# Kernel optimization log

Measured on AMD Instinct MI355X. Metric: run time of the kernel, lower is better.

## Reference

```python
import jax, jax.numpy as jnp
import numpy as np

N = 100000


def gcn_conv(x, W, b, src, dst, deg_inv_sqrt, n):
    # PyG GCNConv: h = D^{-1/2} (A + I) D^{-1/2} (x W) + b
    h = x @ W  # [N, out]
    norm = deg_inv_sqrt[src] * deg_inv_sqrt[dst]  # [E+N]
    msgs = h[src] * norm[:, None]  # gathered + scaled messages
    out = jax.ops.segment_sum(msgs, dst, num_segments=n)
    return out + b


def _self_loops_and_norm(edge_index, n):
    src, dst = edge_index[0], edge_index[1]
    loop = jnp.arange(n, dtype=edge_index.dtype)
    src = jnp.concatenate([src, loop])
    dst = jnp.concatenate([dst, loop])
    deg = jax.ops.segment_sum(jnp.ones_like(dst, dtype=jnp.float32), dst, num_segments=n)
    deg_inv_sqrt = jnp.where(deg > 0, jax.lax.rsqrt(jnp.maximum(deg, 1.0)), 0.0)
    return src, dst, deg_inv_sqrt


def setup_inputs() -> dict:
    key = jax.random.key(0)
    k1, k2, k3, k4 = jax.random.split(key, 4)
    nfeat, nhid, nclass = 512, 256, 40
    E = 3200000
    x = jax.random.normal(k1, (N, nfeat), dtype=jnp.float32)
    edge_index = jax.random.randint(k2, (2, E), 0, N, dtype=jnp.int64)
    # Glorot-style init for GCNConv weights, zero bias (PyG default)
    W1 = jax.random.normal(k3, (nfeat, nhid), dtype=jnp.float32) / np.sqrt(nfeat)
    b1 = jnp.zeros((nhid,), dtype=jnp.float32)
    W2 = jax.random.normal(k4, (nhid, nclass), dtype=jnp.float32) / np.sqrt(nhid)
    b2 = jnp.zeros((nclass,), dtype=jnp.float32)
    return {"x": x, "W1": W1, "b1": b1, "W2": W2, "b2": b2, "edge_index": edge_index}


def reference(x, W1, b1, W2, b2, edge_index):
    src, dst, dis = _self_loops_and_norm(edge_index, N)
    h = gcn_conv(x, W1, b1, src, dst, dis, N)
    h = jax.nn.relu(h)
    # dropout(p=0.5) is identity in eval mode
    h = gcn_conv(h, W2, b2, src, dst, dis, N)
    return jax.nn.log_softmax(h, axis=1)
```

## Files before the change

### kernel.cpp

```cpp
#include <hip/hip_runtime.h>
#include <math.h>

#define NFEAT 512
#define NHID  256
#define NCLASS 40
#define NBUCK 782
#define BCAP  5120
#define PCHUNK 8192

typedef __attribute__((ext_vector_type(8))) short short8;
typedef __attribute__((ext_vector_type(4))) float f32x4;


__device__ __forceinline__ float bflo(unsigned u) {
    union { unsigned i; float f; } x; x.i = u << 16; return x.f;
}
__device__ __forceinline__ float bfhi(unsigned u) {
    union { unsigned i; float f; } x; x.i = u & 0xffff0000u; return x.f;
}
__device__ __forceinline__ unsigned short f2bf(float f) {
    union { float f; unsigned i; } x; x.f = f;
    unsigned r = x.i + 0x7fffu + ((x.i >> 16) & 1u);
    return (unsigned short)(r >> 16);
}
__device__ __forceinline__ float bf2f(unsigned short h) {
    union { unsigned i; float f; } x; x.i = (unsigned)h << 16; return x.f;
}
__device__ __forceinline__ unsigned pack2(float a, float b) {
    return (unsigned)f2bf(a) | ((unsigned)f2bf(b) << 16);
}


__global__ __launch_bounds__(256) void partcast_k(const float* __restrict__ W1,
                                                  unsigned short* __restrict__ WTsw,
                                                  const float* __restrict__ W2,
                                                  unsigned short* __restrict__ WT2,
                                                  const int* __restrict__ ei,
                                                  int* bucketCnt,
                                                  unsigned* __restrict__ binned, int E) {
    __shared__ unsigned staged[PCHUNK];
    __shared__ int hist[NBUCK];
    __shared__ int lofs[NBUCK];
    __shared__ int sbase[NBUCK];
    __shared__ int lcur[NBUCK];
    __shared__ int wsum[256];
    int bid = blockIdx.x;
    int t = threadIdx.x;
    if (bid < 64) {
        int tid = bid * 256 + t;
        int nn = tid >> 6;
        int k8 = tid & 63;
        unsigned short buf[8];
#pragma unroll
        for (int j = 0; j < 8; ++j)
            buf[j] = f2bf(W1[(size_t)(k8 * 8 + j) * NHID + nn]);
        size_t dst = ((size_t)((nn >> 4) * 16 + (k8 >> 2)) * 64 +
                      (k8 & 3) * 16 + (nn & 15)) * 8;
        *(uint4*)(WTsw + dst) = *(const uint4*)buf;
        return;
    }
    if (bid == 64) {
        for (int idx = t; idx < 96 * 256; idx += 256) {
            int j2 = idx >> 8;
            int k = idx & 255;
            int j = (j2 < 48) ? j2 : j2 - 48;
            float v = (j < NCLASS) ? W2[k * NCLASS + j] : 0.f;
            unsigned short hi = f2bf(v);
            WT2[idx] = (j2 < 48) ? hi : f2bf(v - bf2f(hi));
        }
        return;
    }
    int pb = bid - 65;
    int beg = pb * PCHUNK;
    int end = beg + PCHUNK; if (end > E) end = E;

    for (int b = t; b < NBUCK; b += 256) hist[b] = 0;
    __syncthreads();
    for (int e = beg + t; e < end; e += 256) {
        int d = ei[(size_t)E + e];
        atomicAdd(&hist[d >> 7], 1);
    }
    __syncthreads();
    int v[4];
    int s0 = 0;
#pragma unroll
    for (int r = 0; r < 4; ++r) {
        int idx = t * 4 + r;
        v[r] = (idx < NBUCK) ? hist[idx] : 0;
        s0 += v[r];
    }
    wsum[t] = s0;
    __syncthreads();
    for (int off = 1; off < 256; off <<= 1) {
        int add = (t >= off) ? wsum[t - off] : 0;
        __syncthreads();
        wsum[t] += add;
        __syncthreads();
    }
    int excl = wsum[t] - s0;
#pragma unroll
    for (int r = 0; r < 4; ++r) {
        int idx = t * 4 + r;
        if (idx < NBUCK) { lofs[idx] = excl; lcur[idx] = excl; }
        excl += v[r];
    }
    __syncthreads();
    for (int b = t; b < NBUCK; b += 256) {
        int h = hist[b];
        if (h) sbase[b] = atomicAdd(&bucketCnt[b], h);
    }
    for (int e = beg + t; e < end; e += 256) {
        int s = ei[e];
        int d = ei[(size_t)E + e];
        int b = d >> 7;
        int p = atomicAdd(&lcur[b], 1);
        staged[p] = ((unsigned)s << 7) | (unsigned)(d & 127);
    }
    __syncthreads();
    int w = t >> 6, lane = t & 63;
    for (int b = w; b < NBUCK; b += 4) {
        int h = hist[b];
        if (!h) continue;
        int lo = lofs[b];
        size_t gb = (size_t)b * BCAP + sbase[b];
        for (int l = lane; l < h; l += 64)
            binned[gb + l] = staged[lo + l];
    }
}


__global__ __launch_bounds__(1024) void bscan_k(const int* __restrict__ bucketCnt,
                                                int* __restrict__ bbase,
                                                int* __restrict__ offs, int n, int E) {
    __shared__ int sd[1024];
    int t = threadIdx.x;
    int v = (t < NBUCK) ? bucketCnt[t] : 0;
    sd[t] = v;
    __syncthreads();
    for (int off = 1; off < 1024; off <<= 1) {
        int add = (t >= off) ? sd[t - off] : 0;
        __syncthreads();
        sd[t] += add;
        __syncthreads();
    }
    if (t < NBUCK) bbase[t] = sd[t] - v;
    if (t == 0) offs[n] = E;
}


__global__ __launch_bounds__(512) void fill2_k(const unsigned* __restrict__ binned,
                                               const int* __restrict__ bucketCnt,
                                               const int* __restrict__ bbase,
                                               int* __restrict__ offs,
                                               float* __restrict__ dis,
                                               int* __restrict__ csrs, int n) {
    __shared__ int h128[128];
    __shared__ int sd[128];
    __shared__ int lcur[128];
    int b = blockIdx.x;
    int t = threadIdx.x;
    int node0 = b << 7;
    int cbt = bucketCnt[b];
    size_t base_in = (size_t)b * BCAP;
    int gbase = bbase[b];
    if (t < 128) h128[t] = 0;
    __syncthreads();
    for (int e = t; e < cbt; e += 512) {
        unsigned u = binned[base_in + e];
        atomicAdd(&h128[u & 127], 1);
    }
    __syncthreads();
    int v = (t < 128) ? h128[t] : 0;
    if (t < 128) sd[t] = v;
    __syncthreads();
    for (int off = 1; off < 128; off <<= 1) {
        int add = (t < 128 && t >= off) ? sd[t - off] : 0;
        __syncthreads();
        if (t < 128) sd[t] += add;
        __syncthreads();
    }
    if (t < 128) {
        int excl = sd[t] - v;
        int nd = node0 + t;
        if (nd < n) {
            offs[nd] = gbase + excl;
            dis[nd] = rsqrtf((float)v + 1.0f);
        }
        lcur[t] = gbase + excl;
    }
    __syncthreads();
    for (int e = t; e < cbt; e += 512) {
        unsigned u = binned[base_in + e];
        int pos = atomicAdd(&lcur[u & 127], 1);
        csrs[pos] = (int)(u >> 7);
    }
}


__global__ __launch_bounds__(512) void gemm1_k(const float* __restrict__ X,
                                               const unsigned short* __restrict__ WTsw,
                                               const float* __restrict__ dis,
                                               unsigned short* __restrict__ H, int M) {
    __shared__ unsigned short as[128][72];
    int t = threadIdx.x;
    int lane = t & 63;
    int w = t >> 6;
    int wm = w >> 2;
    int wn = w & 3;
    int m0 = blockIdx.x * 128;
    int quad = lane >> 4;
    int r16 = lane & 15;

    f32x4 acc[4][4];
#pragma unroll
    for (int a = 0; a < 4; ++a)
#pragma unroll
        for (int b = 0; b < 4; ++b) acc[a][b] = (f32x4){0.f, 0.f, 0.f, 0.f};

    for (int k0 = 0; k0 < NFEAT; k0 += 64) {
        {
            int m = t >> 2;
            int c = (t & 3) * 16;
            int gi = m0 + m;
            float4 v0, v1, v2, v3;
            if (gi < M) {
                const float4* p = (const float4*)(X + (size_t)gi * NFEAT + k0 + c);
                v0 = p[0]; v1 = p[1]; v2 = p[2]; v3 = p[3];
            } else {
                v0 = v1 = v2 = v3 = make_float4(0.f, 0.f, 0.f, 0.f);
            }
            uint4 p0, p1;
            p0.x = pack2(v0.x, v0.y); p0.y = pack2(v0.z, v0.w);
            p0.z = pack2(v1.x, v1.y); p0.w = pack2(v1.z, v1.w);
            p1.x = pack2(v2.x, v2.y); p1.y = pack2(v2.z, v2.w);
            p1.z = pack2(v3.x, v3.y); p1.w = pack2(v3.z, v3.w);
            *(uint4*)&as[m][c] = p0;
            *(uint4*)&as[m][c + 8] = p1;
        }
        __syncthreads();
        int kb0 = k0 >> 5;
#pragma unroll
        for (int ks = 0; ks < 2; ++ks) {
            int kblk = kb0 + ks;
            short8 af[4], bfr[4];
#pragma unroll
            for (int sm = 0; sm < 4; ++sm)
                af[sm] = *(const short8*)&as[wm * 64 + sm * 16 + r16][ks * 32 + quad * 8];
#pragma unroll
            for (int sn = 0; sn < 4; ++sn)
                bfr[sn] = *(const short8*)(WTsw +
                    ((size_t)((wn * 4 + sn) * 16 + kblk) * 64 + lane) * 8);
#pragma unroll
            for (int sm = 0; sm < 4; ++sm)
#pragma unroll
                for (int sn = 0; sn < 4; ++sn)
                    acc[sm][sn] = __builtin_amdgcn_mfma_f32_16x16x32_bf16(
                        af[sm], bfr[sn], acc[sm][sn], 0, 0, 0);
        }
        __syncthreads();
    }
#pragma unroll
    for (int sm = 0; sm < 4; ++sm) {
#pragma unroll
        for (int rr = 0; rr < 4; ++rr) {
            int row = m0 + wm * 64 + sm * 16 + quad * 4 + rr;
            if (row < M) {
                float dsc = dis[row];
#pragma unroll
                for (int sn = 0; sn < 4; ++sn) {
                    int col = wn * 64 + sn * 16 + r16;
                    H[(size_t)row * NHID + col] = f2bf(acc[sm][sn][rr] * dsc);
                }
            }
        }
    }
}


__global__ __launch_bounds__(256) void agg1h_k(const unsigned short* __restrict__ Hb,
                                               const int* __restrict__ offs,
                                               const int* __restrict__ csrs,
                                               const float* __restrict__ dis,
                                               const float* __restrict__ b1,
                                               unsigned short* __restrict__ outb,
                                               int n, int f0u) {
    int lane = threadIdx.x & 63;
    int i = blockIdx.x * 4 + (threadIdx.x >> 6);
    if (i >= n) return;
    const unsigned* Hv = (const unsigned*)Hb;
    int col = f0u + lane;
    float a0 = 0.f, a1 = 0.f;
    int beg = offs[i], end = offs[i + 1];
    int e = beg;
    {
        int c[16]; unsigned g[16];
        for (; e + 16 <= end; e += 16) {
#pragma unroll
            for (int u = 0; u < 16; ++u) c[u] = csrs[e + u];
#pragma unroll
            for (int u = 0; u < 16; ++u) g[u] = Hv[(size_t)c[u] * 128 + col];
#pragma unroll
            for (int u = 0; u < 16; ++u) {
                a0 += bflo(g[u]); a1 += bfhi(g[u]);
            }
        }
        if (e < end) {
#pragma unroll
            for (int u = 0; u < 16; ++u)
                c[u] = (e + u < end) ? csrs[e + u] : i;
#pragma unroll
            for (int u = 0; u < 16; ++u) g[u] = Hv[(size_t)c[u] * 128 + col];
#pragma unroll
            for (int u = 0; u < 16; ++u) {
                float sel = (e + u < end) ? 1.f : 0.f;
                a0 = fmaf(sel, bflo(g[u]), a0); a1 = fmaf(sel, bfhi(g[u]), a1);
            }
        }
    }
    unsigned v = Hv[(size_t)i * 128 + col];
    a0 += bflo(v); a1 += bfhi(v);
    float di = dis[i];
    float2 bb = ((const float2*)b1)[col];
    a0 = fmaxf(fmaf(a0, di, bb.x), 0.f);
    a1 = fmaxf(fmaf(a1, di, bb.y), 0.f);
    ((unsigned*)outb)[(size_t)i * 128 + col] = pack2(a0, a1);
}


__global__ __launch_bounds__(256) void gemm2_k(const unsigned short* __restrict__ Ab,
                                               const unsigned short* __restrict__ WT2,
                                               const float* __restrict__ dis,
                                               unsigned short* __restrict__ H2b, int M) {
    __shared__ unsigned short wt2s[96][264];
    int t = threadIdx.x;
    int lane = t & 63;
    int w = t >> 6;
    int quad = lane >> 4;
    int r16 = lane & 15;
    for (int idx = t; idx < 96 * 32; idx += 256) {
        int r = idx >> 5;
        int c = idx & 31;
        *(uint4*)&wt2s[r][c * 8] = ((const uint4*)(WT2 + (size_t)r * 256))[c];
    }
    __syncthreads();
    int row0 = blockIdx.x * 64 + w * 16;
    int gr = row0 + r16;
    f32x4 acc[3];
#pragma unroll
    for (int sn = 0; sn < 3; ++sn) acc[sn] = (f32x4){0.f, 0.f, 0.f, 0.f};
#pragma unroll
    for (int ks = 0; ks < 8; ++ks) {
        short8 af;
        if (gr < M)
            af = *(const short8*)(Ab + (size_t)gr * NHID + ks * 32 + quad * 8);
        else
            af = (short8){0, 0, 0, 0, 0, 0, 0, 0};
#pragma unroll
        for (int sn = 0; sn < 3; ++sn) {
            short8 bhi = *(const short8*)&wt2s[sn * 16 + r16][ks * 32 + quad * 8];
            short8 blo = *(const short8*)&wt2s[48 + sn * 16 + r16][ks * 32 + quad * 8];
            acc[sn] = __builtin_amdgcn_mfma_f32_16x16x32_bf16(af, bhi, acc[sn], 0, 0, 0);
            acc[sn] = __builtin_amdgcn_mfma_f32_16x16x32_bf16(af, blo, acc[sn], 0, 0, 0);
        }
    }
#pragma unroll
    for (int rr = 0; rr < 4; ++rr) {
        int row = row0 + quad * 4 + rr;
        if (row < M) {
            float dsc = dis[row];
#pragma unroll
            for (int sn = 0; sn < 3; ++sn)
                H2b[(size_t)row * 64 + sn * 16 + r16] = f2bf(acc[sn][rr] * dsc);
        }
    }
    if (lane < 32) {
        int row = row0 + r16;
        if (row < M)
            *(uint4*)&H2b[(size_t)row * 64 + 48 + (lane >> 4) * 8] =
                make_uint4(0u, 0u, 0u, 0u);
    }
}


__global__ __launch_bounds__(256) void agg2_k(const unsigned short* __restrict__ H2b,
                                              const int* __restrict__ offs,
                                              const int* __restrict__ csrs,
                                              const float* __restrict__ dis,
                                              const float* __restrict__ b2,
                                              float* __restrict__ out, int n) {
    int lane = threadIdx.x & 63;
    int i = blockIdx.x * 4 + (threadIdx.x >> 6);
    if (i >= n) return;
    const uint2* Hv = (const uint2*)H2b;
    int slot = lane >> 4;
    int r16 = lane & 15;
    float a0 = 0.f, a1 = 0.f, a2 = 0.f, a3 = 0.f;
    int beg = offs[i], end = offs[i + 1];
    int e = beg;
    {
        int c[8]; uint2 g[8];
        for (; e + 32 <= end; e += 32) {
#pragma unroll
            for (int u = 0; u < 8; ++u) c[u] = csrs[e + u * 4 + slot];
#pragma unroll
            for (int u = 0; u < 8; ++u) g[u] = Hv[(size_t)c[u] * 16 + r16];
#pragma unroll
            for (int u = 0; u < 8; ++u) {
                a0 += bflo(g[u].x); a1 += bfhi(g[u].x);
                a2 += bflo(g[u].y); a3 += bfhi(g[u].y);
            }
        }
        if (e < end) {
#pragma unroll
            for (int u = 0; u < 8; ++u) {
                int idx = e + u * 4 + slot;
                c[u] = (idx < end) ? csrs[idx] : i;
            }
#pragma unroll
            for (int u = 0; u < 8; ++u) g[u] = Hv[(size_t)c[u] * 16 + r16];
#pragma unroll
            for (int u = 0; u < 8; ++u) {
                float sel = (e + u * 4 + slot < end) ? 1.f : 0.f;
                a0 = fmaf(sel, bflo(g[u].x), a0); a1 = fmaf(sel, bfhi(g[u].x), a1);
                a2 = fmaf(sel, bflo(g[u].y), a2); a3 = fmaf(sel, bfhi(g[u].y), a3);
            }
        }
    }
    if (slot == 0) {
        uint2 v = Hv[(size_t)i * 16 + r16];
        a0 += bflo(v.x); a1 += bfhi(v.x);
        a2 += bflo(v.y); a3 += bfhi(v.y);
    }
    a0 += __shfl_xor(a0, 16, 64); a0 += __shfl_xor(a0, 32, 64);
    a1 += __shfl_xor(a1, 16, 64); a1 += __shfl_xor(a1, 32, 64);
    a2 += __shfl_xor(a2, 16, 64); a2 += __shfl_xor(a2, 32, 64);
    a3 += __shfl_xor(a3, 16, 64); a3 += __shfl_xor(a3, 32, 64);
    float di = dis[i];
    bool act = (r16 < 10);
    float4 bb = act ? ((const float4*)b2)[r16] : make_float4(0.f, 0.f, 0.f, 0.f);
    a0 = fmaf(a0, di, bb.x); a1 = fmaf(a1, di, bb.y);
    a2 = fmaf(a2, di, bb.z); a3 = fmaf(a3, di, bb.w);
    float m = act ? fmaxf(fmaxf(a0, a1), fmaxf(a2, a3)) : -INFINITY;
#pragma unroll
    for (int off = 8; off > 0; off >>= 1) m = fmaxf(m, __shfl_xor(m, off, 16));
    float s = act ? (expf(a0 - m) + expf(a1 - m) + expf(a2 - m) + expf(a3 - m)) : 0.f;
#pragma unroll
    for (int off = 8; off > 0; off >>= 1) s += __shfl_xor(s, off, 16);
    float ls = m + logf(s);
    if (lane < 10) {
        float4 o = make_float4(a0 - ls, a1 - ls, a2 - ls, a3 - ls);
        ((float4*)(out + (size_t)i * NCLASS))[lane] = o;
    }
}


extern "C" void kernel_launch(void* const* d_in, const int* in_sizes, int n_in,
                              void* d_out, int out_size, void* d_ws, size_t ws_size,
                              hipStream_t stream) {
    const float* x  = (const float*)d_in[0];
    const float* W1 = (const float*)d_in[1];
    const float* b1 = (const float*)d_in[2];
    const float* W2 = (const float*)d_in[3];
    const float* b2 = (const float*)d_in[4];
    const int*   ei = (const int*)d_in[5];

    const int N = in_sizes[0] / NFEAT;
    const int E = in_sizes[5] / 2;

    size_t off = 0;
    auto alloc = [&](size_t bytes) { size_t o = off; off += (bytes + 255) & ~(size_t)255; return o; };
    char* ws = (char*)d_ws;
    int*            offs    = (int*)           (ws + alloc((size_t)(N + 1) * 4));
    float*          dis     = (float*)         (ws + alloc((size_t)N * 4));
    int*            bcnt    = (int*)           (ws + alloc((size_t)NBUCK * 4));
    int*            bbase   = (int*)           (ws + alloc((size_t)NBUCK * 4));
    unsigned*       binned  = (unsigned*)      (ws + alloc((size_t)NBUCK * BCAP * 4));
    int*            csrs    = (int*)           (ws + alloc((size_t)E * 4));
    unsigned short* wTsw    = (unsigned short*)(ws + alloc((size_t)NFEAT * NHID * 2));
    unsigned short* wT2     = (unsigned short*)(ws + alloc((size_t)96 * 256 * 2));
    unsigned short* h1b     = (unsigned short*)(ws + alloc((size_t)N * NHID * 2));
    unsigned short* a1b     = (unsigned short*)(ws + alloc((size_t)N * NHID * 2));
    unsigned short* h2b     = (unsigned short*)(ws + alloc((size_t)N * 64 * 2));
    float*          out     = (float*)d_out;

    int npart = (E + PCHUNK - 1) / PCHUNK;

    hipMemsetAsync(bcnt, 0, (size_t)NBUCK * 4, stream);
    partcast_k<<<65 + npart, 256, 0, stream>>>(W1, wTsw, W2, wT2, ei, bcnt, binned, E);
    bscan_k<<<1, 1024, 0, stream>>>(bcnt, bbase, offs, N, E);
    fill2_k<<<NBUCK, 512, 0, stream>>>(binned, bcnt, bbase, offs, dis, csrs, N);
    gemm1_k<<<(N + 127) / 128, 512, 0, stream>>>(x, wTsw, dis, h1b, N);
    agg1h_k<<<(N + 3) / 4, 256, 0, stream>>>(h1b, offs, csrs, dis, b1, a1b, N, 0);
    agg1h_k<<<(N + 3) / 4, 256, 0, stream>>>(h1b, offs, csrs, dis, b1, a1b, N, 64);
    gemm2_k<<<(N + 63) / 64, 256, 0, stream>>>(a1b, wT2, dis, h2b, N);
    agg2_k<<<(N + 3) / 4, 256, 0, stream>>>(h2b, offs, csrs, dis, b2, out, N);
}
```

Before: 710.5 us.

## Sub-sort CSR neighbors into source-index ranges for gather locality

The CSR build now splits each destination node's neighbor list into 8 source-index ranges (by src/12500), storing 8 offsets per node. The first-layer aggregation walks the ranges in order, so concurrent warps tend to gather from similar regions of H and get better L2/MALL locality. The cost is a larger offset array, extra per-range loop overhead with partial 8-wide tails in agg1, and a hardcoded 12500 divisor that assumes N=100000.

```diff
diff --git a/kernel.cpp b/kernel.cpp
--- a/kernel.cpp
+++ b/kernel.cpp
@@ -7,6 +7,7 @@
 #define NBUCK 782
 #define BCAP  5120
 #define PCHUNK 8192
+#define NRANGE 8
 
 typedef __attribute__((ext_vector_type(8))) short short8;
 typedef __attribute__((ext_vector_type(4))) float f32x4;
@@ -131,7 +132,7 @@
 
 __global__ __launch_bounds__(1024) void bscan_k(const int* __restrict__ bucketCnt,
                                                 int* __restrict__ bbase,
-                                                int* __restrict__ offs, int n, int E) {
+                                                int* __restrict__ offsR, int n, int E) {
     __shared__ int sd[1024];
     int t = threadIdx.x;
     int v = (t < NBUCK) ? bucketCnt[t] : 0;
@@ -144,55 +145,66 @@
         __syncthreads();
     }
     if (t < NBUCK) bbase[t] = sd[t] - v;
-    if (t == 0) offs[n] = E;
+    if (t == 0) offsR[(size_t)n * NRANGE] = E;
 }
 
 
 __global__ __launch_bounds__(512) void fill2_k(const unsigned* __restrict__ binned,
                                                const int* __restrict__ bucketCnt,
                                                const int* __restrict__ bbase,
-                                               int* __restrict__ offs,
+                                               int* __restrict__ offsR,
                                                float* __restrict__ dis,
                                                int* __restrict__ csrs, int n) {
-    __shared__ int h128[128];
-    __shared__ int sd[128];
-    __shared__ int lcur[128];
+    __shared__ int h[1024];
+    __shared__ int sd[512];
+    __shared__ int lcur[1024];
     int b = blockIdx.x;
     int t = threadIdx.x;
     int node0 = b << 7;
     int cbt = bucketCnt[b];
     size_t base_in = (size_t)b * BCAP;
     int gbase = bbase[b];
-    if (t < 128) h128[t] = 0;
+    h[t] = 0; h[t + 512] = 0;
     __syncthreads();
     for (int e = t; e < cbt; e += 512) {
         unsigned u = binned[base_in + e];
-        atomicAdd(&h128[u & 127], 1);
-    }
-    __syncthreads();
-    int v = (t < 128) ? h128[t] : 0;
-    if (t < 128) sd[t] = v;
-    __syncthreads();
-    for (int off = 1; off < 128; off <<= 1) {
-        int add = (t < 128 && t >= off) ? sd[t - off] : 0;
-        __syncthreads();
-        if (t < 128) sd[t] += add;
-        __syncthreads();
-    }
+        int s = (int)(u >> 7);
+        int r = s / 12500;
+        atomicAdd(&h[((u & 127) << 3) + r], 1);
+    }
+    __syncthreads();
+    int v0 = h[t * 2], v1 = h[t * 2 + 1];
+    int s2 = v0 + v1;
+    sd[t] = s2;
+    __syncthreads();
+    for (int off = 1; off < 512; off <<= 1) {
+        int add = (t >= off) ? sd[t - off] : 0;
+        __syncthreads();
+        sd[t] += add;
+        __syncthreads();
+    }
+    int excl = sd[t] - s2;
+    lcur[t * 2] = gbase + excl;
+    lcur[t * 2 + 1] = gbase + excl + v0;
+    __syncthreads();
+    offsR[(size_t)(node0 << 3) + t] = lcur[t];
+    offsR[(size_t)(node0 << 3) + t + 512] = lcur[t + 512];
     if (t < 128) {
-        int excl = sd[t] - v;
         int nd = node0 + t;
         if (nd < n) {
-            offs[nd] = gbase + excl;
-            dis[nd] = rsqrtf((float)v + 1.0f);
-        }
-        lcur[t] = gbase + excl;
+            int deg = 0;
+#pragma unroll
+            for (int r = 0; r < 8; ++r) deg += h[(t << 3) + r];
+            dis[nd] = rsqrtf((float)deg + 1.0f);
+        }
     }
     __syncthreads();
     for (int e = t; e < cbt; e += 512) {
         unsigned u = binned[base_in + e];
-        int pos = atomicAdd(&lcur[u & 127], 1);
-        csrs[pos] = (int)(u >> 7);
+        int s = (int)(u >> 7);
+        int r = s / 12500;
+        int pos = atomicAdd(&lcur[((u & 127) << 3) + r], 1);
+        csrs[pos] = s;
     }
 }
 
@@ -278,7 +290,7 @@
 
 
 __global__ __launch_bounds__(256) void agg1h_k(const unsigned short* __restrict__ Hb,
-                                               const int* __restrict__ offs,
+                                               const int* __restrict__ offsR,
                                                const int* __restrict__ csrs,
                                                const float* __restrict__ dis,
                                                const float* __restrict__ b1,
@@ -290,30 +302,23 @@
     const unsigned* Hv = (const unsigned*)Hb;
     int col = f0u + lane;
     float a0 = 0.f, a1 = 0.f;
-    int beg = offs[i], end = offs[i + 1];
-    int e = beg;
-    {
-        int c[16]; unsigned g[16];
-        for (; e + 16 <= end; e += 16) {
-#pragma unroll
-            for (int u = 0; u < 16; ++u) c[u] = csrs[e + u];
-#pragma unroll
-            for (int u = 0; u < 16; ++u) g[u] = Hv[(size_t)c[u] * 128 + col];
-#pragma unroll
-            for (int u = 0; u < 16; ++u) {
-                a0 += bflo(g[u]); a1 += bfhi(g[u]);
-            }
-        }
-        if (e < end) {
-#pragma unroll
-            for (int u = 0; u < 16; ++u)
-                c[u] = (e + u < end) ? csrs[e + u] : i;
-#pragma unroll
-            for (int u = 0; u < 16; ++u) g[u] = Hv[(size_t)c[u] * 128 + col];
-#pragma unroll
-            for (int u = 0; u < 16; ++u) {
-                float sel = (e + u < end) ? 1.f : 0.f;
-                a0 = fmaf(sel, bflo(g[u]), a0); a1 = fmaf(sel, bfhi(g[u]), a1);
+    int o[9];
+#pragma unroll
+    for (int r = 0; r < 9; ++r) o[r] = offsR[(size_t)i * 8 + r];
+    int c[8]; unsigned g[8];
+#pragma unroll 1
+    for (int r = 0; r < 8; ++r) {
+        int e1 = o[r + 1];
+        for (int e = o[r]; e < e1; e += 8) {
+#pragma unroll
+            for (int u = 0; u < 8; ++u) c[u] = (e + u < e1) ? csrs[e + u] : i;
+#pragma unroll
+            for (int u = 0; u < 8; ++u) g[u] = Hv[(size_t)c[u] * 128 + col];
+#pragma unroll
+            for (int u = 0; u < 8; ++u) {
+                float sel = (e + u < e1) ? 1.f : 0.f;
+                a0 = fmaf(sel, bflo(g[u]), a0);
+                a1 = fmaf(sel, bfhi(g[u]), a1);
             }
         }
     }
@@ -383,7 +388,7 @@
 
 
 __global__ __launch_bounds__(256) void agg2_k(const unsigned short* __restrict__ H2b,
-                                              const int* __restrict__ offs,
+                                              const int* __restrict__ offsR,
                                               const int* __restrict__ csrs,
                                               const float* __restrict__ dis,
                                               const float* __restrict__ b2,
@@ -395,7 +400,8 @@
     int slot = lane >> 4;
     int r16 = lane & 15;
     float a0 = 0.f, a1 = 0.f, a2 = 0.f, a3 = 0.f;
-    int beg = offs[i], end = offs[i + 1];
+    int beg = offsR[(size_t)i * 8];
+    int end = offsR[(size_t)(i + 1) * 8];
     int e = beg;
     {
         int c[8]; uint2 g[8];
@@ -470,7 +476,7 @@
     size_t off = 0;
     auto alloc = [&](size_t bytes) { size_t o = off; off += (bytes + 255) & ~(size_t)255; return o; };
     char* ws = (char*)d_ws;
-    int*            offs    = (int*)           (ws + alloc((size_t)(N + 1) * 4));
+    int*            offsR   = (int*)           (ws + alloc(((size_t)NBUCK * 128 * 8 + 16) * 4));
     float*          dis     = (float*)         (ws + alloc((size_t)N * 4));
     int*            bcnt    = (int*)           (ws + alloc((size_t)NBUCK * 4));
     int*            bbase   = (int*)           (ws + alloc((size_t)NBUCK * 4));
@@ -487,11 +493,11 @@
 
     hipMemsetAsync(bcnt, 0, (size_t)NBUCK * 4, stream);
     partcast_k<<<65 + npart, 256, 0, stream>>>(W1, wTsw, W2, wT2, ei, bcnt, binned, E);
-    bscan_k<<<1, 1024, 0, stream>>>(bcnt, bbase, offs, N, E);
-    fill2_k<<<NBUCK, 512, 0, stream>>>(binned, bcnt, bbase, offs, dis, csrs, N);
+    bscan_k<<<1, 1024, 0, stream>>>(bcnt, bbase, offsR, N, E);
+    fill2_k<<<NBUCK, 512, 0, stream>>>(binned, bcnt, bbase, offsR, dis, csrs, N);
     gemm1_k<<<(N + 127) / 128, 512, 0, stream>>>(x, wTsw, dis, h1b, N);
-    agg1h_k<<<(N + 3) / 4, 256, 0, stream>>>(h1b, offs, csrs, dis, b1, a1b, N, 0);
-    agg1h_k<<<(N + 3) / 4, 256, 0, stream>>>(h1b, offs, csrs, dis, b1, a1b, N, 64);
+    agg1h_k<<<(N + 3) / 4, 256, 0, stream>>>(h1b, offsR, csrs, dis, b1, a1b, N, 0);
+    agg1h_k<<<(N + 3) / 4, 256, 0, stream>>>(h1b, offsR, csrs, dis, b1, a1b, N, 64);
     gemm2_k<<<(N + 63) / 64, 256, 0, stream>>>(a1b, wT2, dis, h2b, N);
-    agg2_k<<<(N + 3) / 4, 256, 0, stream>>>(h2b, offs, csrs, dis, b2, out, N);
-}
+    agg2_k<<<(N + 3) / 4, 256, 0, stream>>>(h2b, offsR, csrs, dis, b2, out, N);
+}
```

After: 771.6 us. 8.6% more time.
